# Kernel tuning notes

Hardware: AMD Instinct MI355X
Metric: run time of the kernel (lower is better)

## Reference

```python
import jax, jax.numpy as jnp
import numpy as np

HEADS = 8
DIM_HEAD = 128
SCALE = DIM_HEAD ** -0.5
EPS = 1e-5


def layer_norm(t, w, b):
    mu = t.mean(-1, keepdims=True)
    var = ((t - mu) ** 2).mean(-1, keepdims=True)
    return (t - mu) * jax.lax.rsqrt(var + EPS) * w + b


def setup_inputs() -> dict:
    key = jax.random.key(0)
    ks = jax.random.split(key, 8)
    b, n, dim = 4, 1024, 1024
    inner = HEADS * DIM_HEAD  # 1024
    w = 0.02
    return {
        "x": jax.random.normal(ks[0], (b, n, dim), jnp.float32),
        "cond_info": jax.random.normal(ks[1], (b, n, dim), jnp.float32),
        "ref": jax.random.normal(ks[2], (b, n, dim), jnp.float32),
        "ln_w": jnp.ones((dim,), jnp.float32),
        "ln_b": jnp.zeros((dim,), jnp.float32),
        "cln_w": jnp.ones((dim,), jnp.float32),
        "cln_b": jnp.zeros((dim,), jnp.float32),
        "Wk": jax.random.normal(ks[3], (3 * dim, inner), jnp.float32) * w,
        "Wv": jax.random.normal(ks[4], (2 * dim, inner), jnp.float32) * w,
        "Wo": jax.random.normal(ks[5], (inner, dim), jnp.float32) * w,
        "bo": jnp.zeros((dim,), jnp.float32),
        "th_w": jax.random.normal(ks[6], (HEADS, HEADS), jnp.float32) * 0.3,
        "cth_w": jax.random.normal(ks[7], (HEADS, HEADS), jnp.float32) * 0.3,
    }


def reference(x, cond_info, ref, ln_w, ln_b, cln_w, cln_b, Wk, Wv, Wo, bo, th_w, cth_w):
    b, n, _ = x.shape
    h, d = HEADS, DIM_HEAD
    xn = layer_norm(x, ln_w, ln_b)
    rn = layer_norm(ref, ln_w, ln_b)
    cn = layer_norm(cond_info, cln_w, cln_b)
    # projections (y_to_q output is unused in the original forward; omitted)
    cond = jnp.concatenate([xn, cn, rn], axis=-1) @ Wk   # [b, n, h*d]
    refv = jnp.concatenate([xn, rn], axis=-1) @ Wv       # [b, n, h*d]
    split = lambda t: t.reshape(b, n, h, d).transpose(0, 2, 1, 3)  # b h n d
    cond, refv = split(cond), split(refv)
    sim = jnp.einsum('bhid,bhjd->bhij', cond, refv) * SCALE
    attn = jax.nn.softmax(sim, axis=-1)           # row softmax
    context_attn = jax.nn.softmax(sim, axis=-2)   # column softmax
    # talking heads: 1x1 conv over head dim, weight [out_h, in_h]
    attn = jnp.einsum('gh,bhij->bgij', th_w, attn)
    context_attn = jnp.einsum('gh,bhij->bgij', cth_w, context_attn)
    out = jnp.einsum('bhij,bhjd->bhid', attn, refv)
    context_out = jnp.einsum('bhji,bhjd->bhid', context_attn, cond)
    merge = lambda t: t.transpose(0, 2, 1, 3).reshape(b, n, h * d)
    out = merge(out) @ Wo + bo
    context_out = merge(context_out)
    return out, context_out
```

## Files before the change

### kernel.cpp

```cpp
#include <hip/hip_runtime.h>
#include <hip/hip_bf16.h>
#include <stdint.h>

typedef unsigned short u16;
typedef __attribute__((ext_vector_type(8))) short bf16x8;
typedef __attribute__((ext_vector_type(4))) float f32x4;

#define HEADS 8
#define DHEAD 128
#define NSEQ 1024
#define BATCH 4
#define DIM 1024
#define ATT_SCALE 0.088388347648318447f

static __device__ __forceinline__ float bf2f(u16 u){
  union { unsigned int i; float f; } c; c.i = ((unsigned int)u) << 16; return c.f;
}
static __device__ __forceinline__ u16 f2bf(float f){
  union { float f; unsigned int i; } c; c.f = f;
  unsigned int x = c.i;
  return (u16)((x + 0x7fffu + ((x >> 16) & 1u)) >> 16);
}

static __device__ __forceinline__ void gload_lds16(const void* g, void* l){
  __builtin_amdgcn_global_load_lds((__attribute__((address_space(1))) void*)(g),
                                   (__attribute__((address_space(3))) void*)(l),
                                   16, 0, 0);
}

__global__ __launch_bounds__(256)
void ln3_kernel(const float* __restrict__ x, const float* __restrict__ ref,
                const float* __restrict__ cinfo,
                const float* __restrict__ ln_w, const float* __restrict__ ln_b,
                const float* __restrict__ cln_w, const float* __restrict__ cln_b,
                u16* __restrict__ xn, u16* __restrict__ rn, u16* __restrict__ cn)
{
  const int z = blockIdx.y;
  const float* src = (z==0) ? x : (z==1) ? ref : cinfo;
  const float* w   = (z==2) ? cln_w : ln_w;
  const float* b   = (z==2) ? cln_b : ln_b;
  u16* out         = (z==0) ? xn : (z==1) ? rn : cn;

  const int row = blockIdx.x;
  const int t = threadIdx.x;
  const float* xr = src + (size_t)row * DIM;
  float4 v4 = *(const float4*)(xr + t*4);
  float v[4] = {v4.x, v4.y, v4.z, v4.w};
  float s = v[0]+v[1]+v[2]+v[3];
  __shared__ float red[256];
  red[t] = s; __syncthreads();
  for (int o=128;o;o>>=1){ if (t<o) red[t]+=red[t+o]; __syncthreads(); }
  const float mean = red[0] * (1.0f/DIM);
  __syncthreads();
  s = 0.f;
#pragma unroll
  for (int i=0;i<4;i++){ float d = v[i]-mean; s += d*d; }
  red[t] = s; __syncthreads();
  for (int o=128;o;o>>=1){ if (t<o) red[t]+=red[t+o]; __syncthreads(); }
  const float rstd = rsqrtf(red[0]*(1.0f/DIM) + 1e-5f);
  float4 w4 = *(const float4*)(w + t*4);
  float4 b4 = *(const float4*)(b + t*4);
  float wv[4] = {w4.x, w4.y, w4.z, w4.w};
  float bv[4] = {b4.x, b4.y, b4.z, b4.w};
  union { uint2 u; u16 s[4]; } ov;
#pragma unroll
  for (int i=0;i<4;i++)
    ov.s[i] = f2bf((v[i]-mean)*rstd*wv[i] + bv[i]);
  *(uint2*)(out + (size_t)row*DIM + t*4) = ov.u;
}

__global__ __launch_bounds__(256)
void wcvt_kernel(const float* __restrict__ Wk, const float* __restrict__ Wv,
                 const float* __restrict__ Wo,
                 u16* __restrict__ WkT, u16* __restrict__ WvT, u16* __restrict__ WoT)
{
  const int z = blockIdx.z;
  const int K = (z==0) ? 3072 : (z==1) ? 2048 : 1024;
  if ((int)blockIdx.x*32 >= K) return;
  const float* W = (z==0) ? Wk : (z==1) ? Wv : Wo;
  u16* WT = (z==0) ? WkT : (z==1) ? WvT : WoT;
  __shared__ float tile[32][33];
  const int k0 = blockIdx.x*32, n0 = blockIdx.y*32;
  const int t = threadIdx.x, tc = t&31, tr = t>>5;
#pragma unroll
  for (int p=0;p<4;p++)
    tile[tr+p*8][tc] = W[(size_t)(k0+tr+p*8)*DIM + n0+tc];
  __syncthreads();
#pragma unroll
  for (int p=0;p<4;p++)
    WT[(size_t)(n0+tr+p*8)*K + k0+tc] = f2bf(tile[tc][tr+p*8]);
}

__global__ __launch_bounds__(256)
void gemm_kernel(const u16* __restrict__ A0, const u16* __restrict__ A1,
                 const u16* __restrict__ A2, const u16* __restrict__ A0b,
                 const u16* __restrict__ A1b,
                 const u16* __restrict__ B1, const u16* __restrict__ B2,
                 void* __restrict__ Cv, void* __restrict__ Cv2,
                 const float* __restrict__ bias,
                 int K1, int K2, int lda, int ldb1, int ldb2, int ldc,
                 long a_plane, long b_plane, long c_plane,
                 int epi1, int epi2, int z_split, float alpha)
{
  __shared__ __attribute__((aligned(16))) u16 sA[2][4096];
  __shared__ __attribute__((aligned(16))) u16 sB[2][4096];
  const int t = threadIdx.x;
  const int m0 = blockIdx.y*128, n0 = blockIdx.x*128;
  const int zz = blockIdx.z;
  const bool side = (zz >= z_split);
  const int z = side ? (zz - z_split) : zz;
  const u16* a0 = (side ? A0b : A0) + (size_t)z*a_plane;
  const u16* a1 = (side ? A1b : A1) + (size_t)z*a_plane;
  const u16* a2 = A2 + (size_t)z*a_plane;
  const u16* bB = (side ? B2 : B1) + (size_t)z*b_plane;
  void* Cp = side ? Cv2 : Cv;
  const int EPI = side ? epi2 : epi1;
  const int K   = side ? K2 : K1;
  const int ldb = side ? ldb2 : ldb1;

  const int wave = t>>6, lane = t&63;
  const int wm = (wave>>1)*64, wn = (wave&1)*64;
  const int lm = lane&15, q = lane>>4;

  const f32x4 zero4 = {0.f,0.f,0.f,0.f};
  f32x4 acc[4][4];
#pragma unroll
  for (int i=0;i<4;i++)
#pragma unroll
    for (int j=0;j<4;j++) acc[i][j] = zero4;

  const int arowblk = wave*32;

  const int KT = K >> 5;

  auto issueA = [&](int kt, int buf){
    const int kg = kt<<5, seg = kg>>10, ka = kg&1023;
    const u16* Ap = (seg==0) ? a0 : (seg==1 ? a1 : a2);
#pragma unroll
    for (int rr=0; rr<2; ++rr){
      const int rb = arowblk + rr*16;
      gload_lds16(Ap + (size_t)(m0+rb+lm)*lda + (ka + q*8), &sA[buf][rb*32]);
    }
  };
  auto issueB = [&](int kt, int buf){
    const int kg = kt<<5;
#pragma unroll
    for (int rr=0; rr<2; ++rr){
      const int rb = arowblk + rr*16;
      gload_lds16(bB + (size_t)(n0+rb+lm)*ldb + (kg + q*8), &sB[buf][rb*32]);
    }
  };

  issueA(0, 0);
  issueB(0, 0);

  int cur = 0;
  for (int kt=0; kt<KT; ++kt){
    __syncthreads();
    if (kt+1 < KT){
      issueA(kt+1, cur^1);
      issueB(kt+1, cur^1);
    }
    bf16x8 af[4], bfr[4];
#pragma unroll
    for (int f=0; f<4; ++f){
      af[f]  = *(const bf16x8*)&sA[cur][((wm>>4)+f)*512 + lane*8];
      bfr[f] = *(const bf16x8*)&sB[cur][((wn>>4)+f)*512 + lane*8];
    }
#pragma unroll
    for (int fm=0; fm<4; ++fm)
#pragma unroll
      for (int fn=0; fn<4; ++fn)
        acc[fm][fn] = __builtin_amdgcn_mfma_f32_16x16x32_bf16(af[fm], bfr[fn], acc[fm][fn], 0, 0, 0);
    cur ^= 1;
  }

#pragma unroll
  for (int fm=0; fm<4; ++fm){
#pragma unroll
    for (int fn=0; fn<4; ++fn){
#pragma unroll
      for (int r=0; r<4; ++r){
        const int m = m0 + wm + fm*16 + q*4 + r;
        const int n = n0 + wn + fn*16 + lm;
        float val = acc[fm][fn][r] * alpha;
        if (EPI == 0){
          ((u16*)Cp)[(size_t)z*c_plane + (size_t)m*ldc + n] = f2bf(val);
        } else if (EPI == 1){
          ((u16*)Cp)[((size_t)(z>>3)*NSEQ + m)*DIM + (size_t)(z&7)*DHEAD + n] = f2bf(val);
        } else if (EPI == 2){
          ((float*)Cp)[(size_t)m*ldc + n] = val + bias[n];
        } else if (EPI == 3){
          ((u16*)Cp)[(size_t)(((m>>10)*HEADS + (n>>7))*NSEQ + (m&1023))*DHEAD + (n&127)] = f2bf(val);
        } else {
          ((float*)Cp)[((size_t)(z>>3)*NSEQ + m)*DIM + (size_t)(z&7)*DHEAD + n] = val;
        }
      }
    }
  }
}

__global__ __launch_bounds__(256)
void gemm8_kernel(const u16* __restrict__ A, const u16* __restrict__ B,
                  float* __restrict__ P)
{
  __shared__ __attribute__((aligned(16))) u16 sA[2][4096];
  __shared__ __attribute__((aligned(16))) u16 sB[2][4096];
  const int t = threadIdx.x;
  const int bid = blockIdx.x;
  const int w = (bid & 7)*128 + (bid >> 3);
  const int x = w & 7;
  const int y = (w >> 3) & 31;
  const int s = w >> 8;
  const int m0 = y*128, n0 = x*128, k0 = s*256;

  const int wave = t>>6, lane = t&63;
  const int wm = (wave>>1)*64, wn = (wave&1)*64;
  const int lm = lane&15, q = lane>>4;

  const f32x4 zero4 = {0.f,0.f,0.f,0.f};
  f32x4 acc[4][4];
#pragma unroll
  for (int i=0;i<4;i++)
#pragma unroll
    for (int j=0;j<4;j++) acc[i][j] = zero4;

  const int arowblk = wave*32;

  auto issueA = [&](int kt, int buf){
    const int kg = k0 + (kt<<5);
#pragma unroll
    for (int rr=0; rr<2; ++rr){
      const int rb = arowblk + rr*16;
      gload_lds16(A + (size_t)(m0+rb+lm)*1024 + (kg + q*8), &sA[buf][rb*32]);
    }
  };
  auto issueB = [&](int kt, int buf){
    const int kg = k0 + (kt<<5);
#pragma unroll
    for (int rr=0; rr<2; ++rr){
      const int rb = arowblk + rr*16;
      gload_lds16(B + (size_t)(n0+rb+lm)*1024 + (kg + q*8), &sB[buf][rb*32]);
    }
  };

  issueA(0, 0);
  issueB(0, 0);

  int cur = 0;
  for (int kt=0; kt<8; ++kt){
    __syncthreads();
    if (kt+1 < 8){
      issueA(kt+1, cur^1);
      issueB(kt+1, cur^1);
    }
    bf16x8 af[4], bfr[4];
#pragma unroll
    for (int f=0; f<4; ++f){
      af[f]  = *(const bf16x8*)&sA[cur][((wm>>4)+f)*512 + lane*8];
      bfr[f] = *(const bf16x8*)&sB[cur][((wn>>4)+f)*512 + lane*8];
    }
#pragma unroll
    for (int fm=0; fm<4; ++fm)
#pragma unroll
      for (int fn=0; fn<4; ++fn)
        acc[fm][fn] = __builtin_amdgcn_mfma_f32_16x16x32_bf16(af[fm], bfr[fn], acc[fm][fn], 0, 0, 0);
    cur ^= 1;
  }

  float* Pp = P + (size_t)s*4194304;
#pragma unroll
  for (int fm=0; fm<4; ++fm){
#pragma unroll
    for (int fn=0; fn<4; ++fn){
#pragma unroll
      for (int r=0; r<4; ++r){
        const int m = m0 + wm + fm*16 + q*4 + r;
        const int n = n0 + wn + fn*16 + lm;
        Pp[(size_t)m*1024 + n] = acc[fm][fn][r];
      }
    }
  }
}

__global__ __launch_bounds__(256)
void red8_kernel(const float* __restrict__ P, const float* __restrict__ bias,
                 float* __restrict__ out)
{
  const int idx = blockIdx.x*256 + threadIdx.x;
  const float4* P4 = (const float4*)P;
  float4 a = P4[idx];
  float4 b = P4[idx + 1048576];
  float4 c = P4[idx + 2097152];
  float4 d = P4[idx + 3145728];
  float4 bb = ((const float4*)bias)[idx & 255];
  float4 o;
  o.x = a.x + b.x + c.x + d.x + bb.x;
  o.y = a.y + b.y + c.y + d.y + bb.y;
  o.z = a.z + b.z + c.z + d.z + bb.z;
  o.w = a.w + b.w + c.w + d.w + bb.w;
  ((float4*)out)[idx] = o;
}

__global__ __launch_bounds__(256)
void transpose2_kernel(const u16* __restrict__ cond, const u16* __restrict__ refv,
                       u16* __restrict__ condT, u16* __restrict__ refvT)
{
  __shared__ u16 tile[32][33];
  const int zz = blockIdx.z;
  const u16* X = (zz < 32) ? cond : refv;
  u16* XT      = (zz < 32) ? condT : refvT;
  const int z = zz & 31;
  const int i0 = blockIdx.y*32, d0 = blockIdx.x*32;
  const int t = threadIdx.x;
  const int tc = t & 31, tr = t >> 5;
  const u16* Xp = X + (size_t)z*NSEQ*DHEAD;
#pragma unroll
  for (int p=0;p<4;p++){
    int i = tr + p*8;
    tile[i][tc] = Xp[(size_t)(i0+i)*DHEAD + d0 + tc];
  }
  __syncthreads();
  u16* Op = XT + (size_t)z*DHEAD*NSEQ;
#pragma unroll
  for (int p=0;p<4;p++){
    int d = tr + p*8;
    Op[(size_t)(d0+d)*NSEQ + i0 + tc] = tile[tc][d];
  }
}

__global__ __launch_bounds__(256)
void stats_kernel(const u16* __restrict__ sim,
                  float* __restrict__ rmax, float* __restrict__ rrcp,
                  float* __restrict__ cmax, float* __restrict__ crcp)
{
  __shared__ float smx[4][64], ssm[4][64];
  if (blockIdx.x < 8192){
    const int wave = threadIdx.x >> 6, lane = threadIdx.x & 63;
    const int row = blockIdx.x*4 + wave;
    const u16* sr = sim + (size_t)row * NSEQ;
    float v[16]; float m = -1e30f;
#pragma unroll
    for (int c=0;c<16;c++){ v[c] = bf2f(sr[lane + c*64]); m = fmaxf(m, v[c]); }
#pragma unroll
    for (int off=32; off; off>>=1) m = fmaxf(m, __shfl_xor(m, off));
    float s = 0.f;
#pragma unroll
    for (int c=0;c<16;c++) s += __expf(v[c]-m);
#pragma unroll
    for (int off=32; off; off>>=1) s += __shfl_xor(s, off);
    if (lane == 0){ rmax[row] = m; rrcp[row] = 1.0f/s; }
  } else {
    const int t = threadIdx.x;
    const int jl = t & 63, slice = t >> 6;
    const int c = (blockIdx.x - 8192)*64 + jl;
    const int bh = c >> 10, j = c & 1023;
    const u16* sp = sim + (size_t)bh*NSEQ*NSEQ + j + (size_t)(slice*256)*NSEQ;
    float m0=-1e30f, m1=-1e30f, m2=-1e30f, m3=-1e30f;
    for (int i=0;i<256;i+=4){
      m0 = fmaxf(m0, bf2f(sp[(size_t)(i  )*NSEQ]));
      m1 = fmaxf(m1, bf2f(sp[(size_t)(i+1)*NSEQ]));
      m2 = fmaxf(m2, bf2f(sp[(size_t)(i+2)*NSEQ]));
      m3 = fmaxf(m3, bf2f(sp[(size_t)(i+3)*NSEQ]));
    }
    smx[slice][jl] = fmaxf(fmaxf(m0,m1), fmaxf(m2,m3));
    __syncthreads();
    const float M = fmaxf(fmaxf(smx[0][jl], smx[1][jl]),
                          fmaxf(smx[2][jl], smx[3][jl]));
    float s0=0.f, s1=0.f, s2=0.f, s3=0.f;
    for (int i=0;i<256;i+=4){
      s0 += __expf(bf2f(sp[(size_t)(i  )*NSEQ]) - M);
      s1 += __expf(bf2f(sp[(size_t)(i+1)*NSEQ]) - M);
      s2 += __expf(bf2f(sp[(size_t)(i+2)*NSEQ]) - M);
      s3 += __expf(bf2f(sp[(size_t)(i+3)*NSEQ]) - M);
    }
    ssm[slice][jl] = s0+s1+s2+s3;
    __syncthreads();
    if (slice == 0){
      float S = ssm[0][jl] + ssm[1][jl] + ssm[2][jl] + ssm[3][jl];
      cmax[c] = M; crcp[c] = 1.0f/S;
    }
  }
}

__global__ __launch_bounds__(256)
void mix_kernel(u16* simam,
                const float* __restrict__ rmax, const float* __restrict__ rrcp,
                const float* __restrict__ cmax, const float* __restrict__ crcp,
                const float* __restrict__ thw, const float* __restrict__ cthw,
                u16* __restrict__ cmT)
{
  __shared__ float s_th[64], s_cth[64];
  __shared__ u16 s_cm[8][32][33];
  const int t = threadIdx.x;
  if (t < 64){ s_th[t] = thw[t]; s_cth[t] = cthw[t]; }
  __syncthreads();
  const int b = blockIdx.z, i0 = blockIdx.y*32, j0 = blockIdx.x*32;
  const int tj = t & 31, ti = t >> 5;
  for (int p=0;p<4;p++){
    const int i = ti + p*8;
    float a[8], c[8];
#pragma unroll
    for (int h=0;h<8;h++){
      const int bh = b*8 + h;
      const float v = bf2f(simam[((size_t)bh*NSEQ + (i0+i))*NSEQ + j0 + tj]);
      a[h] = __expf(v - rmax[(size_t)bh*NSEQ + i0+i]) * rrcp[(size_t)bh*NSEQ + i0+i];
      c[h] = __expf(v - cmax[(size_t)bh*NSEQ + j0+tj]) * crcp[(size_t)bh*NSEQ + j0+tj];
    }
#pragma unroll
    for (int g=0;g<8;g++){
      float sa = 0.f, sc = 0.f;
#pragma unroll
      for (int h=0;h<8;h++){ sa += s_th[g*8+h]*a[h]; sc += s_cth[g*8+h]*c[h]; }
      simam[((size_t)(b*8+g)*NSEQ + (i0+i))*NSEQ + j0 + tj] = f2bf(sa);
      s_cm[g][i][tj] = f2bf(sc);
    }
  }
  __syncthreads();
#pragma unroll
  for (int g=0;g<8;g++){
#pragma unroll
    for (int p=0;p<4;p++){
      const int j = ti + p*8;
      cmT[((size_t)(b*8+g)*NSEQ + (j0+j))*NSEQ + i0 + tj] = s_cm[g][tj][j];
    }
  }
}

extern "C" void kernel_launch(void* const* d_in, const int* in_sizes, int n_in,
                              void* d_out, int out_size, void* d_ws, size_t ws_size,
                              hipStream_t stream)
{
  const float* x     = (const float*)d_in[0];
  const float* cinfo = (const float*)d_in[1];
  const float* ref   = (const float*)d_in[2];
  const float* ln_w  = (const float*)d_in[3];
  const float* ln_b  = (const float*)d_in[4];
  const float* cln_w = (const float*)d_in[5];
  const float* cln_b = (const float*)d_in[6];
  const float* Wk    = (const float*)d_in[7];
  const float* Wv    = (const float*)d_in[8];
  const float* Wo    = (const float*)d_in[9];
  const float* bo    = (const float*)d_in[10];
  const float* thw   = (const float*)d_in[11];
  const float* cthw  = (const float*)d_in[12];
  float* out = (float*)d_out;

  char* ws = (char*)d_ws;
  u16* xn    = (u16*)(ws + 0);
  u16* cn    = (u16*)(ws + 8388608);
  u16* rn    = (u16*)(ws + 16777216);
  u16* cond  = (u16*)(ws + 25165824);
  u16* refv  = (u16*)(ws + 33554432);
  u16* condT = (u16*)(ws + 41943040);
  u16* refvT = (u16*)(ws + 50331648);
  u16* sim   = (u16*)(ws + 58720256);
  u16* cmT   = (u16*)(ws + 125829120);
  u16* WkT   = (u16*)(ws + 192937984);
  u16* WvT   = (u16*)(ws + 199229440);
  u16* WoT   = (u16*)(ws + 203423744);
  float* rmax = (float*)(ws + 8388608);
  float* rrcp = (float*)(ws + 8388608 + 131072);
  float* cmax = (float*)(ws + 8388608 + 262144);
  float* crcp = (float*)(ws + 8388608 + 393216);
  u16* out_pre = (u16*)(ws + 0);

  ln3_kernel<<<dim3(4096,3), 256, 0, stream>>>(x, ref, cinfo, ln_w, ln_b,
                                               cln_w, cln_b, xn, rn, cn);

  wcvt_kernel<<<dim3(96,32,3), 256, 0, stream>>>(Wk, Wv, Wo, WkT, WvT, WoT);

  gemm_kernel<<<dim3(8,32,2), 256, 0, stream>>>(
      xn, cn, rn, xn, rn, WkT, WvT, cond, refv, nullptr,
      3072, 2048, DIM, 3072, 2048, 0, 0, 0, 0, 3, 3, 1, 1.0f);

  transpose2_kernel<<<dim3(4,32,64), 256, 0, stream>>>(cond, refv, condT, refvT);

  gemm_kernel<<<dim3(8,8,32), 256, 0, stream>>>(
      cond, cond, cond, cond, cond, refv, refv, sim, sim, nullptr,
      DHEAD, DHEAD, DHEAD, DHEAD, DHEAD, NSEQ,
      (long)NSEQ*DHEAD, (long)NSEQ*DHEAD, (long)NSEQ*NSEQ, 0, 0, 1000000, ATT_SCALE);

  stats_kernel<<<8704, 256, 0, stream>>>(sim, rmax, rrcp, cmax, crcp);

  mix_kernel<<<dim3(32,32,4), 256, 0, stream>>>(sim, rmax, rrcp, cmax, crcp, thw, cthw, cmT);

  gemm_kernel<<<dim3(1,8,64), 256, 0, stream>>>(
      sim, sim, sim, cmT, cmT, refvT, condT, out_pre, out + (size_t)BATCH*NSEQ*DIM, nullptr,
      1024, 1024, NSEQ, NSEQ, NSEQ, 0,
      (long)NSEQ*NSEQ, (long)DHEAD*NSEQ, 0, 1, 4, 32, 1.0f);

  gemm8_kernel<<<1024, 256, 0, stream>>>(out_pre, WoT, (float*)sim);
  red8_kernel<<<4096, 256, 0, stream>>>((const float*)sim, bo, out);
}
```

Before: 469.8 us.

## Replace LDS-staged projection GEMM with register-prefetched direct-load MFMA kernel

Adds a dedicated projection GEMM that loads A and B fragments straight from global memory into registers, with a four-deep software prefetch ring, and skips the shared-memory staging and barriers. Each wave computes a 64x64 tile, the concatenated-input segments are selected per k-tile, and the output is written directly in head-split layout. This aims to remove LDS traffic and synchronisation from the large QK projection. In exchange it loses cross-wave reuse through LDS, so global/L2 traffic rises, and the eight fragment buffers add register pressure.

```diff
diff --git a/kernel.cpp b/kernel.cpp
--- a/kernel.cpp
+++ b/kernel.cpp
@@ -89,6 +89,90 @@
 #pragma unroll
   for (int p=0;p<4;p++)
     WT[(size_t)(n0+tr+p*8)*K + k0+tc] = f2bf(tile[tc][tr+p*8]);
+}
+
+__global__ __launch_bounds__(256, 2)
+void gemm64_kernel(const u16* __restrict__ xn, const u16* __restrict__ cn,
+                   const u16* __restrict__ rn,
+                   const u16* __restrict__ WkT, const u16* __restrict__ WvT,
+                   u16* __restrict__ cond, u16* __restrict__ refv)
+{
+  const int t = threadIdx.x;
+  const int wave = t>>6, lane = t&63;
+  const int side = blockIdx.z;
+  const int K    = side ? 2048 : 3072;
+  const int KT   = K >> 5;
+  const u16* B   = side ? WvT : WkT;
+  u16* Cp        = side ? refv : cond;
+  const int m0 = blockIdx.y*128 + (wave>>1)*64;
+  const int n0 = blockIdx.x*128 + (wave&1)*64;
+  const int lm = lane&15, q = lane>>4;
+
+  const f32x4 zero4 = {0.f,0.f,0.f,0.f};
+  f32x4 acc[4][4];
+#pragma unroll
+  for (int i=0;i<4;i++)
+#pragma unroll
+    for (int j=0;j<4;j++) acc[i][j] = zero4;
+
+  auto loadA = [&](int kt, bf16x8* a){
+    const int kg = kt<<5;
+    const int seg = kg>>10;
+    const int ka = (kg&1023) + q*8;
+    const u16* Ap = side ? (seg==0 ? xn : rn)
+                         : (seg==0 ? xn : (seg==1 ? cn : rn));
+#pragma unroll
+    for (int f=0; f<4; ++f)
+      a[f] = *(const bf16x8*)(Ap + (size_t)(m0 + f*16 + lm)*DIM + ka);
+  };
+  auto loadB = [&](int kt, bf16x8* b){
+    const int kb = (kt<<5) + q*8;
+#pragma unroll
+    for (int f=0; f<4; ++f)
+      b[f] = *(const bf16x8*)(B + (size_t)(n0 + f*16 + lm)*(size_t)K + kb);
+  };
+
+#define MMA4(aa, bb)                                                            \
+  do {                                                                          \
+    _Pragma("unroll")                                                           \
+    for (int fm=0; fm<4; ++fm)                                                  \
+      _Pragma("unroll")                                                         \
+      for (int fn=0; fn<4; ++fn)                                                \
+        acc[fm][fn] = __builtin_amdgcn_mfma_f32_16x16x32_bf16(aa[fm], bb[fn],   \
+                                                              acc[fm][fn], 0,0,0);\
+  } while (0)
+
+  bf16x8 aP[4], bP[4], aQ[4], bQ[4], aR[4], bR[4], aS[4], bS[4];
+  loadA(0, aP); loadB(0, bP);
+  loadA(1, aQ); loadB(1, bQ);
+  loadA(2, aR); loadB(2, bR);
+  loadA(3, aS); loadB(3, bS);
+
+  for (int kt=0; kt<KT; kt+=4){
+    MMA4(aP, bP);
+    if (kt+4 < KT){ loadA(kt+4, aP); loadB(kt+4, bP); }
+    MMA4(aQ, bQ);
+    if (kt+5 < KT){ loadA(kt+5, aQ); loadB(kt+5, bQ); }
+    MMA4(aR, bR);
+    if (kt+6 < KT){ loadA(kt+6, aR); loadB(kt+6, bR); }
+    MMA4(aS, bS);
+    if (kt+7 < KT){ loadA(kt+7, aS); loadB(kt+7, bS); }
+  }
+#undef MMA4
+
+#pragma unroll
+  for (int fm=0; fm<4; ++fm){
+#pragma unroll
+    for (int fn=0; fn<4; ++fn){
+#pragma unroll
+      for (int r=0; r<4; ++r){
+        const int m = m0 + fm*16 + q*4 + r;
+        const int n = n0 + fn*16 + lm;
+        Cp[(size_t)(((m>>10)*HEADS + (n>>7))*NSEQ + (m&1023))*DHEAD + (n&127)]
+            = f2bf(acc[fm][fn][r]);
+      }
+    }
+  }
 }
 
 __global__ __launch_bounds__(256)
@@ -244,8 +328,7 @@
     }
   };
 
-  issueA(0, 0);
-  issueB(0, 0);
+  issueA(0, 0); issueB(0, 0);
 
   int cur = 0;
   for (int kt=0; kt<8; ++kt){
@@ -470,9 +553,7 @@
 
   wcvt_kernel<<<dim3(96,32,3), 256, 0, stream>>>(Wk, Wv, Wo, WkT, WvT, WoT);
 
-  gemm_kernel<<<dim3(8,32,2), 256, 0, stream>>>(
-      xn, cn, rn, xn, rn, WkT, WvT, cond, refv, nullptr,
-      3072, 2048, DIM, 3072, 2048, 0, 0, 0, 0, 3, 3, 1, 1.0f);
+  gemm64_kernel<<<dim3(8,32,2), 256, 0, stream>>>(xn, cn, rn, WkT, WvT, cond, refv);
 
   transpose2_kernel<<<dim3(4,32,64), 256, 0, stream>>>(cond, refv, condT, refvT);
 
```

New measurement: 536.2 us. 1.14x slower.
